# Kernel tuning notes

Hardware: AMD Instinct MI355X
Metric: run time of the kernel (lower is better)

## Reference

```python
import jax, jax.numpy as jnp
import numpy as np

B, S, D, H = 4, 2048, 1024, 16
HD = D // H  # head_dim = 64


def setup_inputs() -> dict:
    key = jax.random.key(0)
    kx, kq, kk, kv, ko = jax.random.split(key, 5)
    scale = 1.0 / np.sqrt(D)
    return {
        "x": jax.random.normal(kx, (B, S, D), dtype=jnp.float32),
        "Wq": jax.random.normal(kq, (D, D), dtype=jnp.float32) * scale,
        "Wk": jax.random.normal(kk, (D, D), dtype=jnp.float32) * scale,
        "Wv": jax.random.normal(kv, (D, D), dtype=jnp.float32) * scale,
        "Wo": jax.random.normal(ko, (D, D), dtype=jnp.float32) * scale,
    }


def reference(x, Wq, Wk, Wv, Wo):
    b, s, d = x.shape
    # torch nn.Linear: y = x @ W.T
    q = (x @ Wq.T).reshape(b, s, H, HD).transpose(0, 2, 1, 3)  # [B,H,S,hd]
    k = (x @ Wk.T).reshape(b, s, H, HD).transpose(0, 2, 1, 3)
    v = (x @ Wv.T).reshape(b, s, H, HD).transpose(0, 2, 1, 3)
    attn = jnp.einsum("bhqd,bhkd->bhqk", q, k) / np.sqrt(HD)  # [B,H,S,S]
    attn = jax.nn.softmax(attn, axis=-1)
    out = jnp.einsum("bhqk,bhkd->bhqd", attn, v)  # [B,H,S,hd]
    per_head = out.transpose(0, 2, 1, 3)  # [B,S,H,hd]
    combined = per_head.reshape(b, s, d)
    projected = combined @ Wo.T
    return projected, per_head
```

## Files before the change

### kernel.cpp

```cpp
#include <hip/hip_runtime.h>
#include <hip/hip_bf16.h>

#define BB 4
#define SS 2048
#define DD 1024
#define HH 16
#define HDD 64
#define MM (BB*SS)

using bf16x8  = __attribute__((ext_vector_type(8))) short;
using f32x4   = __attribute__((ext_vector_type(4))) float;
using f32x16  = __attribute__((ext_vector_type(16))) float;
using ushort8 = __attribute__((ext_vector_type(8))) unsigned short;
using ushort4v= __attribute__((ext_vector_type(4))) unsigned short;
using uint4v  = __attribute__((ext_vector_type(4))) unsigned int;

#if __has_builtin(__builtin_amdgcn_exp2f)
#define EXP2(x) __builtin_amdgcn_exp2f(x)
#else
#define EXP2(x) exp2f(x)
#endif

__device__ __forceinline__ unsigned short f2bf(float x) {
    unsigned u = __builtin_bit_cast(unsigned, x);
    u += 0x7FFFu + ((u >> 16) & 1u);
    return (unsigned short)(u >> 16);
}

__device__ __forceinline__ unsigned int cvtpk(float lo, float hi) {
    unsigned int r;
    asm("v_cvt_pk_bf16_f32 %0, %1, %2" : "=v"(r) : "v"(lo), "v"(hi));
    return r;
}

#define PSWAP(a, b) asm("v_permlane32_swap_b32 %0, %1" : "+v"(a), "+v"(b))

__device__ __forceinline__ void load_lds16(const void* g, void* l) {
    __builtin_amdgcn_global_load_lds(
        (const __attribute__((address_space(1))) void*)g,
        (__attribute__((address_space(3))) void*)l, 16, 0, 0);
}

__global__ __launch_bounds__(256) void cvt_bf16(const float* __restrict__ in,
                                                unsigned short* __restrict__ out,
                                                int n, float scale) {
    int i = (blockIdx.x * 256 + threadIdx.x) * 8;
    if (i >= n) return;
    float4 a = *(const float4*)(in + i);
    float4 b = *(const float4*)(in + i + 4);
    ushort8 r;
    r[0] = f2bf(a.x*scale); r[1] = f2bf(a.y*scale); r[2] = f2bf(a.z*scale); r[3] = f2bf(a.w*scale);
    r[4] = f2bf(b.x*scale); r[5] = f2bf(b.y*scale); r[6] = f2bf(b.z*scale); r[7] = f2bf(b.w*scale);
    *(ushort8*)(out + i) = r;
}

__global__ __launch_bounds__(256) void cvt_weights(const float* __restrict__ wq,
                                                   const float* __restrict__ wk,
                                                   const float* __restrict__ wv,
                                                   const float* __restrict__ wo,
                                                   unsigned short* __restrict__ oq,
                                                   unsigned short* __restrict__ ok,
                                                   unsigned short* __restrict__ ov,
                                                   unsigned short* __restrict__ oo) {
    const int z = blockIdx.y;
    const float* src = z == 0 ? wq : z == 1 ? wk : z == 2 ? wv : wo;
    unsigned short* dst = z == 0 ? oq : z == 1 ? ok : z == 2 ? ov : oo;
    const float scale = z == 0 ? 0.18033688011112042f : 1.0f;
    int i = (blockIdx.x * 256 + threadIdx.x) * 8;
    float4 a = *(const float4*)(src + i);
    float4 b = *(const float4*)(src + i + 4);
    ushort8 r;
    r[0] = f2bf(a.x*scale); r[1] = f2bf(a.y*scale); r[2] = f2bf(a.z*scale); r[3] = f2bf(a.w*scale);
    r[4] = f2bf(b.x*scale); r[5] = f2bf(b.y*scale); r[6] = f2bf(b.z*scale); r[7] = f2bf(b.w*scale);
    *(ushort8*)(dst + i) = r;
}

template<int LAYOUT>
__device__ __forceinline__ void gemm_body(const unsigned short* __restrict__ A,
                                          const unsigned short* __restrict__ W,
                                          void* __restrict__ Cout,
                                          unsigned short* As, unsigned short* Bs) {
    const int t    = threadIdx.x;
    const int lane = t & 63, wid = t >> 6;
    const int wr   = wid >> 1, wc = wid & 1;
    const int lrow = lane & 15, lkg = lane >> 4;
    const int lid  = blockIdx.y * 8 + blockIdx.x;
    const int ord  = (lid & 7) * 64 + (lid >> 3);
    const int row0 = (ord >> 3) * 128, col0 = (ord & 7) * 128;

    f32x4 acc[4][4];
    #pragma unroll
    for (int m = 0; m < 4; ++m)
        #pragma unroll
        for (int n = 0; n < 4; ++n) acc[m][n] = (f32x4){0.f, 0.f, 0.f, 0.f};

    const int c0 = t, c1 = t + 256;
    const unsigned short* Ag0 = A + (size_t)(row0 + (c0 >> 2)) * DD + (c0 & 3) * 8;
    const unsigned short* Ag1 = A + (size_t)(row0 + (c1 >> 2)) * DD + (c1 & 3) * 8;
    const unsigned short* Wg0 = W + (size_t)(col0 + (c0 >> 2)) * DD + (c0 & 3) * 8;
    const unsigned short* Wg1 = W + (size_t)(col0 + (c1 >> 2)) * DD + (c1 & 3) * 8;

    auto stage = [&](int buf, int k0) {
        load_lds16(Ag0 + k0, &As[buf*128*32 + c0 * 8]);
        load_lds16(Ag1 + k0, &As[buf*128*32 + c1 * 8]);
        load_lds16(Wg0 + k0, &Bs[buf*128*32 + c0 * 8]);
        load_lds16(Wg1 + k0, &Bs[buf*128*32 + c1 * 8]);
    };

    stage(0, 0);
    __syncthreads();
    for (int kt = 0; kt < DD / 32; ++kt) {
        const int cur = kt & 1;
        if (kt + 1 < DD / 32) stage(cur ^ 1, (kt + 1) * 32);
        bf16x8 af[4], bfr[4];
        #pragma unroll
        for (int m = 0; m < 4; ++m)
            af[m] = *(const bf16x8*)&As[cur*128*32 + (wr*64 + m*16 + lrow) * 32 + lkg*8];
        #pragma unroll
        for (int n = 0; n < 4; ++n)
            bfr[n] = *(const bf16x8*)&Bs[cur*128*32 + (wc*64 + n*16 + lrow) * 32 + lkg*8];
        __builtin_amdgcn_s_setprio(1);
        #pragma unroll
        for (int m = 0; m < 4; ++m)
            #pragma unroll
            for (int n = 0; n < 4; ++n)
                acc[m][n] = __builtin_amdgcn_mfma_f32_16x16x32_bf16(af[m], bfr[n], acc[m][n], 0, 0, 0);
        __builtin_amdgcn_s_setprio(0);
        __syncthreads();
    }

    #pragma unroll
    for (int m = 0; m < 4; ++m) {
        #pragma unroll
        for (int n = 0; n < 4; ++n) {
            if (LAYOUT == 2) {
                int gm0 = row0 + wr*64 + m*16 + lkg*4;
                int gn  = col0 + wc*64 + n*16 + lrow;
                int b_ = gm0 >> 11, s0 = gm0 & 2047;
                int h_ = gn >> 6,  hd = gn & 63;
                ushort4v hv;
                hv[0] = f2bf(acc[m][n][0]); hv[1] = f2bf(acc[m][n][1]);
                hv[2] = f2bf(acc[m][n][2]); hv[3] = f2bf(acc[m][n][3]);
                *(ushort4v*)&((unsigned short*)Cout)[(((size_t)b_*HH + h_)*HDD + hd)*SS + s0] = hv;
            } else {
                #pragma unroll
                for (int j = 0; j < 4; ++j) {
                    int gm = row0 + wr*64 + m*16 + lkg*4 + j;
                    int gn = col0 + wc*64 + n*16 + lrow;
                    float v = acc[m][n][j];
                    if (LAYOUT == 1) {
                        int b_ = gm >> 11, s_ = gm & 2047;
                        int h_ = gn >> 6,  hd = gn & 63;
                        ((unsigned short*)Cout)[(((size_t)b_*HH + h_)*SS + s_)*HDD + hd] = f2bf(v);
                    } else {
                        ((float*)Cout)[(size_t)gm * DD + gn] = v;
                    }
                }
            }
        }
    }
}

__global__ __launch_bounds__(256) void gemm_qkv(const unsigned short* __restrict__ A,
                                                const unsigned short* __restrict__ Wq,
                                                const unsigned short* __restrict__ Wk,
                                                const unsigned short* __restrict__ Wv,
                                                unsigned short* __restrict__ Q,
                                                unsigned short* __restrict__ K,
                                                unsigned short* __restrict__ V) {
    __shared__ unsigned short As[2*128*32];
    __shared__ unsigned short Bs[2*128*32];
    const int z = blockIdx.z;
    if (z == 2)      gemm_body<2>(A, Wv, V, As, Bs);
    else if (z == 1) gemm_body<1>(A, Wk, K, As, Bs);
    else             gemm_body<1>(A, Wq, Q, As, Bs);
}

__global__ __launch_bounds__(256) void gemm_proj(const unsigned short* __restrict__ A,
                                                 const unsigned short* __restrict__ W,
                                                 float* __restrict__ C) {
    __shared__ unsigned short As[2*128*32];
    __shared__ unsigned short Bs[2*128*32];
    gemm_body<0>(A, W, C, As, Bs);
}

__global__ __launch_bounds__(256, 2) void flash_mfma7(const unsigned short* __restrict__ Qg,
                                                      const unsigned short* __restrict__ Kg,
                                                      const unsigned short* __restrict__ Vtg,
                                                      float* __restrict__ outf,
                                                      unsigned short* __restrict__ outb) {
    __shared__ unsigned short Ks[2][64*64];
    __shared__ unsigned short Vs[2][64*64];
    const int t   = threadIdx.x, lane = t & 63, wid = t >> 6;
    const int l31 = lane & 31;
    const int hi  = lane >> 5;
    const int lid = blockIdx.y * 8 + blockIdx.x;
    const int ord = (lid & 7) * 64 + (lid >> 3);
    const int bh  = ord >> 3, b_ = bh >> 4, h_ = bh & 15;
    const int qA  = (ord & 7) * 256 + wid * 32;

    const unsigned short* Qb = Qg  + (size_t)bh * SS * HDD;
    const unsigned short* Kb = Kg  + (size_t)bh * SS * HDD;
    const unsigned short* Vb = Vtg + (size_t)bh * HDD * SS;

    bf16x8 qfA[4], qfB[4];
    #pragma unroll
    for (int ks = 0; ks < 4; ++ks) {
        qfA[ks] = *(const bf16x8*)&Qb[(size_t)(qA + l31) * HDD + ks*16 + hi*8];
        qfB[ks] = *(const bf16x8*)&Qb[(size_t)(qA + 128 + l31) * HDD + ks*16 + hi*8];
    }

    f32x16 osA0, osA1, osB0, osB1, sumA, sumB, z;
    #pragma unroll
    for (int r = 0; r < 16; ++r) {
        osA0[r] = 0.f; osA1[r] = 0.f; osB0[r] = 0.f; osB1[r] = 0.f;
        sumA[r] = 0.f; sumB[r] = 0.f; z[r] = 0.f;
    }

    bf16x8 onesf;
    #pragma unroll
    for (int e = 0; e < 8; ++e) onesf[e] = (short)0x3F80;

    const int c0 = t, c1 = t + 256;
    const unsigned sb0 = ((unsigned)(c0 << 4)) ^ ((((unsigned)c0 >> 3) & 7u) << 4);
    const unsigned sb1 = ((unsigned)(c1 << 4)) ^ ((((unsigned)c1 >> 3) & 7u) << 4);
    const unsigned xs  = ((unsigned)(l31 & 7)) << 4;

    bf16x8 kr0, kr1, vr0, vr1;
    kr0 = *(const bf16x8*)&Kb[8*c0];
    kr1 = *(const bf16x8*)&Kb[8*c1];
    vr0 = *(const bf16x8*)&Vb[(size_t)(c0 >> 3) * SS + (c0 & 7) * 8];
    vr1 = *(const bf16x8*)&Vb[(size_t)(c1 >> 3) * SS + (c1 & 7) * 8];
    *(bf16x8*)((char*)&Ks[0][0] + sb0) = kr0;
    *(bf16x8*)((char*)&Ks[0][0] + sb1) = kr1;
    *(bf16x8*)((char*)&Vs[0][0] + sb0) = vr0;
    *(bf16x8*)((char*)&Vs[0][0] + sb1) = vr1;
    __syncthreads();

    for (int kt = 0; kt < SS/64; ++kt) {
        const int cur = kt & 1;
        if (kt + 1 < SS/64) {
            kr0 = *(const bf16x8*)&Kb[(size_t)(kt+1)*4096 + 8*c0];
            kr1 = *(const bf16x8*)&Kb[(size_t)(kt+1)*4096 + 8*c1];
            vr0 = *(const bf16x8*)&Vb[(size_t)(c0 >> 3) * SS + (kt+1)*64 + (c0 & 7) * 8];
            vr1 = *(const bf16x8*)&Vb[(size_t)(c1 >> 3) * SS + (kt+1)*64 + (c1 & 7) * 8];
        }
        const char* Kc = (const char*)&Ks[cur][0];
        const char* Vc = (const char*)&Vs[cur][0];

        f32x16 saA0, saA1, saB0, saB1;
        __builtin_amdgcn_s_setprio(1);
        #pragma unroll
        for (int ks = 0; ks < 4; ++ks) {
            const unsigned cb = ks*32 + hi*16;
            bf16x8 kf0 = *(const bf16x8*)(Kc + (((unsigned)(l31*128)      + cb) ^ xs));
            bf16x8 kf1 = *(const bf16x8*)(Kc + (((unsigned)((32+l31)*128) + cb) ^ xs));
            if (ks == 0) {
                saA0 = __builtin_amdgcn_mfma_f32_32x32x16_bf16(kf0, qfA[0], z, 0, 0, 0);
                saA1 = __builtin_amdgcn_mfma_f32_32x32x16_bf16(kf1, qfA[0], z, 0, 0, 0);
                saB0 = __builtin_amdgcn_mfma_f32_32x32x16_bf16(kf0, qfB[0], z, 0, 0, 0);
                saB1 = __builtin_amdgcn_mfma_f32_32x32x16_bf16(kf1, qfB[0], z, 0, 0, 0);
            } else {
                saA0 = __builtin_amdgcn_mfma_f32_32x32x16_bf16(kf0, qfA[ks], saA0, 0, 0, 0);
                saA1 = __builtin_amdgcn_mfma_f32_32x32x16_bf16(kf1, qfA[ks], saA1, 0, 0, 0);
                saB0 = __builtin_amdgcn_mfma_f32_32x32x16_bf16(kf0, qfB[ks], saB0, 0, 0, 0);
                saB1 = __builtin_amdgcn_mfma_f32_32x32x16_bf16(kf1, qfB[ks], saB1, 0, 0, 0);
            }
        }
        __builtin_amdgcn_s_setprio(0);

        unsigned int pkA0[4][2], pkA1[4][2], pkB0[4][2], pkB1[4][2];
        #pragma unroll
        for (int a = 0; a < 4; ++a) {
            #pragma unroll
            for (int h = 0; h < 2; ++h) {
                pkA0[a][h] = cvtpk(EXP2(saA0[4*a + 2*h]), EXP2(saA0[4*a + 2*h + 1]));
                pkA1[a][h] = cvtpk(EXP2(saA1[4*a + 2*h]), EXP2(saA1[4*a + 2*h + 1]));
                pkB0[a][h] = cvtpk(EXP2(saB0[4*a + 2*h]), EXP2(saB0[4*a + 2*h + 1]));
                pkB1[a][h] = cvtpk(EXP2(saB1[4*a + 2*h]), EXP2(saB1[4*a + 2*h + 1]));
            }
        }

        __builtin_amdgcn_s_setprio(1);
        #pragma unroll
        for (int ksg = 0; ksg < 4; ++ksg) {
            const int ks2 = (ksg & 1) * 2;
            unsigned int a0, a1, a2, a3, b0, b1, b2, b3;
            if ((ksg >> 1) == 0) {
                a0 = pkA0[ks2][0]; a2 = pkA0[ks2+1][0]; a1 = pkA0[ks2][1]; a3 = pkA0[ks2+1][1];
                b0 = pkB0[ks2][0]; b2 = pkB0[ks2+1][0]; b1 = pkB0[ks2][1]; b3 = pkB0[ks2+1][1];
            } else {
                a0 = pkA1[ks2][0]; a2 = pkA1[ks2+1][0]; a1 = pkA1[ks2][1]; a3 = pkA1[ks2+1][1];
                b0 = pkB1[ks2][0]; b2 = pkB1[ks2+1][0]; b1 = pkB1[ks2][1]; b3 = pkB1[ks2+1][1];
            }
            PSWAP(a0, a2); PSWAP(a1, a3);
            PSWAP(b0, b2); PSWAP(b1, b3);
            uint4v wa = {a0, a1, a2, a3};
            uint4v wb = {b0, b1, b2, b3};
            bf16x8 pfA = __builtin_bit_cast(bf16x8, wa);
            bf16x8 pfB = __builtin_bit_cast(bf16x8, wb);
            const unsigned cb = ksg*32 + hi*16;
            bf16x8 vf0 = *(const bf16x8*)(Vc + (((unsigned)(l31*128)      + cb) ^ xs));
            bf16x8 vf1 = *(const bf16x8*)(Vc + (((unsigned)((32+l31)*128) + cb) ^ xs));
            osA0 = __builtin_amdgcn_mfma_f32_32x32x16_bf16(vf0, pfA, osA0, 0, 0, 0);
            osA1 = __builtin_amdgcn_mfma_f32_32x32x16_bf16(vf1, pfA, osA1, 0, 0, 0);
            osB0 = __builtin_amdgcn_mfma_f32_32x32x16_bf16(vf0, pfB, osB0, 0, 0, 0);
            osB1 = __builtin_amdgcn_mfma_f32_32x32x16_bf16(vf1, pfB, osB1, 0, 0, 0);
            sumA = __builtin_amdgcn_mfma_f32_32x32x16_bf16(onesf, pfA, sumA, 0, 0, 0);
            sumB = __builtin_amdgcn_mfma_f32_32x32x16_bf16(onesf, pfB, sumB, 0, 0, 0);
        }
        __builtin_amdgcn_s_setprio(0);

        if (kt + 1 < SS/64) {
            char* Kn = (char*)&Ks[cur ^ 1][0];
            char* Vn = (char*)&Vs[cur ^ 1][0];
            *(bf16x8*)(Kn + sb0) = kr0;
            *(bf16x8*)(Kn + sb1) = kr1;
            *(bf16x8*)(Vn + sb0) = vr0;
            *(bf16x8*)(Vn + sb1) = vr1;
        }
        __syncthreads();
    }

    #pragma unroll
    for (int g = 0; g < 2; ++g) {
        const float invl = 1.0f / (g == 0 ? sumA[0] : sumB[0]);
        const int   s_   = qA + (g ? 128 : 0) + l31;
        float*          po = outf + (((size_t)b_ * SS + s_) * HH + h_) * HDD;
        unsigned short* pb = outb + (((size_t)b_ * SS + s_) * HH + h_) * HDD;
        #pragma unroll
        for (int a = 0; a < 4; ++a) {
            {
                const f32x16& o = g == 0 ? osA0 : osB0;
                const int d0 = 8*a + 4*hi;
                float4 v; v.x = o[4*a+0]*invl; v.y = o[4*a+1]*invl;
                          v.z = o[4*a+2]*invl; v.w = o[4*a+3]*invl;
                *(float4*)&po[d0] = v;
                ushort4v hv; hv[0]=f2bf(v.x); hv[1]=f2bf(v.y); hv[2]=f2bf(v.z); hv[3]=f2bf(v.w);
                *(ushort4v*)&pb[d0] = hv;
            }
            {
                const f32x16& o = g == 0 ? osA1 : osB1;
                const int d0 = 32 + 8*a + 4*hi;
                float4 v; v.x = o[4*a+0]*invl; v.y = o[4*a+1]*invl;
                          v.z = o[4*a+2]*invl; v.w = o[4*a+3]*invl;
                *(float4*)&po[d0] = v;
                ushort4v hv; hv[0]=f2bf(v.x); hv[1]=f2bf(v.y); hv[2]=f2bf(v.z); hv[3]=f2bf(v.w);
                *(ushort4v*)&pb[d0] = hv;
            }
        }
    }
}

extern "C" void kernel_launch(void* const* d_in, const int* in_sizes, int n_in,
                              void* d_out, int out_size, void* d_ws, size_t ws_size,
                              hipStream_t stream) {
    const float* x  = (const float*)d_in[0];
    const float* Wq = (const float*)d_in[1];
    const float* Wk = (const float*)d_in[2];
    const float* Wv = (const float*)d_in[3];
    const float* Wo = (const float*)d_in[4];
    float* out      = (float*)d_out;
    float* per_head = out + (size_t)MM * DD;

    unsigned short* ws   = (unsigned short*)d_ws;
    const size_t NE = (size_t)MM * DD;
    unsigned short* Qbf  = ws;
    unsigned short* Kbf  = Qbf + NE;
    unsigned short* Vbf  = Kbf + NE;
    unsigned short* xbf  = Vbf + NE;
    unsigned short* wqbf = xbf + NE;
    unsigned short* wkbf = wqbf + (size_t)DD * DD;
    unsigned short* wvbf = wkbf + (size_t)DD * DD;
    unsigned short* wobf = wvbf + (size_t)DD * DD;
    unsigned short* cbf  = wobf + (size_t)DD * DD;

    const int nx = MM * DD;
    const int nw = DD * DD;
    cvt_bf16<<<nx / 2048, 256, 0, stream>>>(x, xbf, nx, 1.0f);
    cvt_weights<<<dim3(nw / 2048, 4), 256, 0, stream>>>(Wq, Wk, Wv, Wo,
                                                        wqbf, wkbf, wvbf, wobf);

    gemm_qkv<<<dim3(DD / 128, MM / 128, 3), 256, 0, stream>>>(xbf, wqbf, wkbf, wvbf,
                                                              Qbf, Kbf, Vbf);

    flash_mfma7<<<dim3(8, BB * HH), 256, 0, stream>>>(Qbf, Kbf, Vbf, per_head, cbf);

    gemm_proj<<<dim3(DD / 128, MM / 128), 256, 0, stream>>>(cbf, wobf, out);
}
```

Baseline: 192.8 us.

## Double flash K/V tile to 128 keys, merge conversion kernels, pack bf16 stores

The flash attention kernel now stages 128 keys of K and V per iteration instead of 64 and processes them as two 64-key halves. This halves the number of barriers and global-to-LDS round trips, at the cost of twice the LDS (64 KB per block), which may limit occupancy at two blocks per CU. The x and weight conversion kernels are merged into one launch. The bf16 output stores now use the packed hardware convert instruction.

Measured after the change: 207.1 us. +7.4%, slower.

```diff
diff --git a/kernel.cpp b/kernel.cpp
--- a/kernel.cpp
+++ b/kernel.cpp
@@ -13,6 +13,7 @@
 using f32x16  = __attribute__((ext_vector_type(16))) float;
 using ushort8 = __attribute__((ext_vector_type(8))) unsigned short;
 using ushort4v= __attribute__((ext_vector_type(4))) unsigned short;
+using uint2v  = __attribute__((ext_vector_type(2))) unsigned int;
 using uint4v  = __attribute__((ext_vector_type(4))) unsigned int;
 
 #if __has_builtin(__builtin_amdgcn_exp2f)
@@ -41,32 +42,27 @@
         (__attribute__((address_space(3))) void*)l, 16, 0, 0);
 }
 
-__global__ __launch_bounds__(256) void cvt_bf16(const float* __restrict__ in,
-                                                unsigned short* __restrict__ out,
-                                                int n, float scale) {
-    int i = (blockIdx.x * 256 + threadIdx.x) * 8;
-    if (i >= n) return;
-    float4 a = *(const float4*)(in + i);
-    float4 b = *(const float4*)(in + i + 4);
-    ushort8 r;
-    r[0] = f2bf(a.x*scale); r[1] = f2bf(a.y*scale); r[2] = f2bf(a.z*scale); r[3] = f2bf(a.w*scale);
-    r[4] = f2bf(b.x*scale); r[5] = f2bf(b.y*scale); r[6] = f2bf(b.z*scale); r[7] = f2bf(b.w*scale);
-    *(ushort8*)(out + i) = r;
-}
-
-__global__ __launch_bounds__(256) void cvt_weights(const float* __restrict__ wq,
-                                                   const float* __restrict__ wk,
-                                                   const float* __restrict__ wv,
-                                                   const float* __restrict__ wo,
-                                                   unsigned short* __restrict__ oq,
-                                                   unsigned short* __restrict__ ok,
-                                                   unsigned short* __restrict__ ov,
-                                                   unsigned short* __restrict__ oo) {
+__global__ __launch_bounds__(256) void cvt_all(const float* __restrict__ x,
+                                               const float* __restrict__ wq,
+                                               const float* __restrict__ wk,
+                                               const float* __restrict__ wv,
+                                               const float* __restrict__ wo,
+                                               unsigned short* __restrict__ ox,
+                                               unsigned short* __restrict__ oq,
+                                               unsigned short* __restrict__ ok,
+                                               unsigned short* __restrict__ ov,
+                                               unsigned short* __restrict__ oo) {
     const int z = blockIdx.y;
-    const float* src = z == 0 ? wq : z == 1 ? wk : z == 2 ? wv : wo;
-    unsigned short* dst = z == 0 ? oq : z == 1 ? ok : z == 2 ? ov : oo;
-    const float scale = z == 0 ? 0.18033688011112042f : 1.0f;
-    int i = (blockIdx.x * 256 + threadIdx.x) * 8;
+    const float* src;
+    unsigned short* dst;
+    float scale = 1.0f;
+    size_t base;
+    if (z < 8)       { src = x;  dst = ox; base = (size_t)z * 512 * 2048; }
+    else if (z == 8) { src = wq; dst = oq; base = 0; scale = 0.18033688011112042f; }
+    else if (z == 9) { src = wk; dst = ok; base = 0; }
+    else if (z == 10){ src = wv; dst = ov; base = 0; }
+    else             { src = wo; dst = oo; base = 0; }
+    size_t i = base + ((size_t)blockIdx.x * 256 + threadIdx.x) * 8;
     float4 a = *(const float4*)(src + i);
     float4 b = *(const float4*)(src + i + 4);
     ushort8 r;
@@ -184,13 +180,13 @@
     gemm_body<0>(A, W, C, As, Bs);
 }
 
-__global__ __launch_bounds__(256, 2) void flash_mfma7(const unsigned short* __restrict__ Qg,
+__global__ __launch_bounds__(256, 2) void flash_mfma8(const unsigned short* __restrict__ Qg,
                                                       const unsigned short* __restrict__ Kg,
                                                       const unsigned short* __restrict__ Vtg,
                                                       float* __restrict__ outf,
                                                       unsigned short* __restrict__ outb) {
-    __shared__ unsigned short Ks[2][64*64];
-    __shared__ unsigned short Vs[2][64*64];
+    __shared__ unsigned short Ks[2][128*64];
+    __shared__ unsigned short Vs[2][2*64*64];
     const int t   = threadIdx.x, lane = t & 63, wid = t >> 6;
     const int l31 = lane & 31;
     const int hi  = lane >> 5;
@@ -221,103 +217,118 @@
     #pragma unroll
     for (int e = 0; e < 8; ++e) onesf[e] = (short)0x3F80;
 
-    const int c0 = t, c1 = t + 256;
-    const unsigned sb0 = ((unsigned)(c0 << 4)) ^ ((((unsigned)c0 >> 3) & 7u) << 4);
-    const unsigned sb1 = ((unsigned)(c1 << 4)) ^ ((((unsigned)c1 >> 3) & 7u) << 4);
-    const unsigned xs  = ((unsigned)(l31 & 7)) << 4;
-
-    bf16x8 kr0, kr1, vr0, vr1;
-    kr0 = *(const bf16x8*)&Kb[8*c0];
-    kr1 = *(const bf16x8*)&Kb[8*c1];
-    vr0 = *(const bf16x8*)&Vb[(size_t)(c0 >> 3) * SS + (c0 & 7) * 8];
-    vr1 = *(const bf16x8*)&Vb[(size_t)(c1 >> 3) * SS + (c1 & 7) * 8];
-    *(bf16x8*)((char*)&Ks[0][0] + sb0) = kr0;
-    *(bf16x8*)((char*)&Ks[0][0] + sb1) = kr1;
-    *(bf16x8*)((char*)&Vs[0][0] + sb0) = vr0;
-    *(bf16x8*)((char*)&Vs[0][0] + sb1) = vr1;
+    unsigned sbK[4], sbV[4];
+    const unsigned short* Kg4[4];
+    const unsigned short* Vg4[4];
+    #pragma unroll
+    for (int i = 0; i < 4; ++i) {
+        const int c = t + 256*i;
+        sbK[i] = ((unsigned)(c << 4)) ^ ((((unsigned)c >> 3) & 7u) << 4);
+        const int half = c >> 9, cv = c & 511;
+        sbV[i] = (unsigned)(half * 8192)
+               + (((unsigned)(cv << 4)) ^ ((((unsigned)cv >> 3) & 7u) << 4));
+        Kg4[i] = Kb + 8*c;
+        Vg4[i] = Vb + (size_t)(cv >> 3) * SS + half*64 + (cv & 7) * 8;
+    }
+    const unsigned xs = ((unsigned)(l31 & 7)) << 4;
+
+    bf16x8 kr[4], vr[4];
+    #pragma unroll
+    for (int i = 0; i < 4; ++i) {
+        kr[i] = *(const bf16x8*)Kg4[i];
+        vr[i] = *(const bf16x8*)Vg4[i];
+        *(bf16x8*)((char*)&Ks[0][0] + sbK[i]) = kr[i];
+        *(bf16x8*)((char*)&Vs[0][0] + sbV[i]) = vr[i];
+    }
     __syncthreads();
 
-    for (int kt = 0; kt < SS/64; ++kt) {
+    for (int kt = 0; kt < SS/128; ++kt) {
         const int cur = kt & 1;
-        if (kt + 1 < SS/64) {
-            kr0 = *(const bf16x8*)&Kb[(size_t)(kt+1)*4096 + 8*c0];
-            kr1 = *(const bf16x8*)&Kb[(size_t)(kt+1)*4096 + 8*c1];
-            vr0 = *(const bf16x8*)&Vb[(size_t)(c0 >> 3) * SS + (kt+1)*64 + (c0 & 7) * 8];
-            vr1 = *(const bf16x8*)&Vb[(size_t)(c1 >> 3) * SS + (kt+1)*64 + (c1 & 7) * 8];
-        }
-        const char* Kc = (const char*)&Ks[cur][0];
-        const char* Vc = (const char*)&Vs[cur][0];
-
-        f32x16 saA0, saA1, saB0, saB1;
-        __builtin_amdgcn_s_setprio(1);
-        #pragma unroll
-        for (int ks = 0; ks < 4; ++ks) {
-            const unsigned cb = ks*32 + hi*16;
-            bf16x8 kf0 = *(const bf16x8*)(Kc + (((unsigned)(l31*128)      + cb) ^ xs));
-            bf16x8 kf1 = *(const bf16x8*)(Kc + (((unsigned)((32+l31)*128) + cb) ^ xs));
-            if (ks == 0) {
-                saA0 = __builtin_amdgcn_mfma_f32_32x32x16_bf16(kf0, qfA[0], z, 0, 0, 0);
-                saA1 = __builtin_amdgcn_mfma_f32_32x32x16_bf16(kf1, qfA[0], z, 0, 0, 0);
-                saB0 = __builtin_amdgcn_mfma_f32_32x32x16_bf16(kf0, qfB[0], z, 0, 0, 0);
-                saB1 = __builtin_amdgcn_mfma_f32_32x32x16_bf16(kf1, qfB[0], z, 0, 0, 0);
-            } else {
-                saA0 = __builtin_amdgcn_mfma_f32_32x32x16_bf16(kf0, qfA[ks], saA0, 0, 0, 0);
-                saA1 = __builtin_amdgcn_mfma_f32_32x32x16_bf16(kf1, qfA[ks], saA1, 0, 0, 0);
-                saB0 = __builtin_amdgcn_mfma_f32_32x32x16_bf16(kf0, qfB[ks], saB0, 0, 0, 0);
-                saB1 = __builtin_amdgcn_mfma_f32_32x32x16_bf16(kf1, qfB[ks], saB1, 0, 0, 0);
-            }
-        }
-        __builtin_amdgcn_s_setprio(0);
-
-        unsigned int pkA0[4][2], pkA1[4][2], pkB0[4][2], pkB1[4][2];
-        #pragma unroll
-        for (int a = 0; a < 4; ++a) {
-            #pragma unroll
-            for (int h = 0; h < 2; ++h) {
-                pkA0[a][h] = cvtpk(EXP2(saA0[4*a + 2*h]), EXP2(saA0[4*a + 2*h + 1]));
-                pkA1[a][h] = cvtpk(EXP2(saA1[4*a + 2*h]), EXP2(saA1[4*a + 2*h + 1]));
-                pkB0[a][h] = cvtpk(EXP2(saB0[4*a + 2*h]), EXP2(saB0[4*a + 2*h + 1]));
-                pkB1[a][h] = cvtpk(EXP2(saB1[4*a + 2*h]), EXP2(saB1[4*a + 2*h + 1]));
-            }
-        }
-
-        __builtin_amdgcn_s_setprio(1);
-        #pragma unroll
-        for (int ksg = 0; ksg < 4; ++ksg) {
-            const int ks2 = (ksg & 1) * 2;
-            unsigned int a0, a1, a2, a3, b0, b1, b2, b3;
-            if ((ksg >> 1) == 0) {
-                a0 = pkA0[ks2][0]; a2 = pkA0[ks2+1][0]; a1 = pkA0[ks2][1]; a3 = pkA0[ks2+1][1];
-                b0 = pkB0[ks2][0]; b2 = pkB0[ks2+1][0]; b1 = pkB0[ks2][1]; b3 = pkB0[ks2+1][1];
-            } else {
-                a0 = pkA1[ks2][0]; a2 = pkA1[ks2+1][0]; a1 = pkA1[ks2][1]; a3 = pkA1[ks2+1][1];
-                b0 = pkB1[ks2][0]; b2 = pkB1[ks2+1][0]; b1 = pkB1[ks2][1]; b3 = pkB1[ks2+1][1];
-            }
-            PSWAP(a0, a2); PSWAP(a1, a3);
-            PSWAP(b0, b2); PSWAP(b1, b3);
-            uint4v wa = {a0, a1, a2, a3};
-            uint4v wb = {b0, b1, b2, b3};
-            bf16x8 pfA = __builtin_bit_cast(bf16x8, wa);
-            bf16x8 pfB = __builtin_bit_cast(bf16x8, wb);
-            const unsigned cb = ksg*32 + hi*16;
-            bf16x8 vf0 = *(const bf16x8*)(Vc + (((unsigned)(l31*128)      + cb) ^ xs));
-            bf16x8 vf1 = *(const bf16x8*)(Vc + (((unsigned)((32+l31)*128) + cb) ^ xs));
-            osA0 = __builtin_amdgcn_mfma_f32_32x32x16_bf16(vf0, pfA, osA0, 0, 0, 0);
-            osA1 = __builtin_amdgcn_mfma_f32_32x32x16_bf16(vf1, pfA, osA1, 0, 0, 0);
-            osB0 = __builtin_amdgcn_mfma_f32_32x32x16_bf16(vf0, pfB, osB0, 0, 0, 0);
-            osB1 = __builtin_amdgcn_mfma_f32_32x32x16_bf16(vf1, pfB, osB1, 0, 0, 0);
-            sumA = __builtin_amdgcn_mfma_f32_32x32x16_bf16(onesf, pfA, sumA, 0, 0, 0);
-            sumB = __builtin_amdgcn_mfma_f32_32x32x16_bf16(onesf, pfB, sumB, 0, 0, 0);
-        }
-        __builtin_amdgcn_s_setprio(0);
-
-        if (kt + 1 < SS/64) {
+        if (kt + 1 < SS/128) {
+            #pragma unroll
+            for (int i = 0; i < 4; ++i) {
+                kr[i] = *(const bf16x8*)(Kg4[i] + (size_t)(kt+1)*8192);
+                vr[i] = *(const bf16x8*)(Vg4[i] + (kt+1)*128);
+            }
+        }
+
+        #pragma unroll
+        for (int h2 = 0; h2 < 2; ++h2) {
+            const char* Kc = (const char*)&Ks[cur][0] + h2 * 8192;
+            const char* Vc = (const char*)&Vs[cur][0] + h2 * 8192;
+
+            f32x16 saA0, saA1, saB0, saB1;
+            __builtin_amdgcn_s_setprio(1);
+            #pragma unroll
+            for (int ks = 0; ks < 4; ++ks) {
+                const unsigned cb = ks*32 + hi*16;
+                bf16x8 kf0 = *(const bf16x8*)(Kc + (((unsigned)(l31*128)      + cb) ^ xs));
+                bf16x8 kf1 = *(const bf16x8*)(Kc + (((unsigned)((32+l31)*128) + cb) ^ xs));
+                if (ks == 0) {
+                    saA0 = __builtin_amdgcn_mfma_f32_32x32x16_bf16(kf0, qfA[0], z, 0, 0, 0);
+                    saA1 = __builtin_amdgcn_mfma_f32_32x32x16_bf16(kf1, qfA[0], z, 0, 0, 0);
+                    saB0 = __builtin_amdgcn_mfma_f32_32x32x16_bf16(kf0, qfB[0], z, 0, 0, 0);
+                    saB1 = __builtin_amdgcn_mfma_f32_32x32x16_bf16(kf1, qfB[0], z, 0, 0, 0);
+                } else {
+                    saA0 = __builtin_amdgcn_mfma_f32_32x32x16_bf16(kf0, qfA[ks], saA0, 0, 0, 0);
+                    saA1 = __builtin_amdgcn_mfma_f32_32x32x16_bf16(kf1, qfA[ks], saA1, 0, 0, 0);
+                    saB0 = __builtin_amdgcn_mfma_f32_32x32x16_bf16(kf0, qfB[ks], saB0, 0, 0, 0);
+                    saB1 = __builtin_amdgcn_mfma_f32_32x32x16_bf16(kf1, qfB[ks], saB1, 0, 0, 0);
+                }
+            }
+            __builtin_amdgcn_s_setprio(0);
+
+            unsigned int pkA0[4][2], pkA1[4][2], pkB0[4][2], pkB1[4][2];
+            #pragma unroll
+            for (int a = 0; a < 4; ++a) {
+                #pragma unroll
+                for (int h = 0; h < 2; ++h) {
+                    pkA0[a][h] = cvtpk(EXP2(saA0[4*a + 2*h]), EXP2(saA0[4*a + 2*h + 1]));
+                    pkA1[a][h] = cvtpk(EXP2(saA1[4*a + 2*h]), EXP2(saA1[4*a + 2*h + 1]));
+                    pkB0[a][h] = cvtpk(EXP2(saB0[4*a + 2*h]), EXP2(saB0[4*a + 2*h + 1]));
+                    pkB1[a][h] = cvtpk(EXP2(saB1[4*a + 2*h]), EXP2(saB1[4*a + 2*h + 1]));
+                }
+            }
+
+            __builtin_amdgcn_s_setprio(1);
+            #pragma unroll
+            for (int ksg = 0; ksg < 4; ++ksg) {
+                const int ks2 = (ksg & 1) * 2;
+                unsigned int a0, a1, a2, a3, b0, b1, b2, b3;
+                if ((ksg >> 1) == 0) {
+                    a0 = pkA0[ks2][0]; a2 = pkA0[ks2+1][0]; a1 = pkA0[ks2][1]; a3 = pkA0[ks2+1][1];
+                    b0 = pkB0[ks2][0]; b2 = pkB0[ks2+1][0]; b1 = pkB0[ks2][1]; b3 = pkB0[ks2+1][1];
+                } else {
+                    a0 = pkA1[ks2][0]; a2 = pkA1[ks2+1][0]; a1 = pkA1[ks2][1]; a3 = pkA1[ks2+1][1];
+                    b0 = pkB1[ks2][0]; b2 = pkB1[ks2+1][0]; b1 = pkB1[ks2][1]; b3 = pkB1[ks2+1][1];
+                }
+                PSWAP(a0, a2); PSWAP(a1, a3);
+                PSWAP(b0, b2); PSWAP(b1, b3);
+                uint4v wa = {a0, a1, a2, a3};
+                uint4v wb = {b0, b1, b2, b3};
+                bf16x8 pfA = __builtin_bit_cast(bf16x8, wa);
+                bf16x8 pfB = __builtin_bit_cast(bf16x8, wb);
+                const unsigned cb = ksg*32 + hi*16;
+                bf16x8 vf0 = *(const bf16x8*)(Vc + (((unsigned)(l31*128)      + cb) ^ xs));
+                bf16x8 vf1 = *(const bf16x8*)(Vc + (((unsigned)((32+l31)*128) + cb) ^ xs));
+                osA0 = __builtin_amdgcn_mfma_f32_32x32x16_bf16(vf0, pfA, osA0, 0, 0, 0);
+                osA1 = __builtin_amdgcn_mfma_f32_32x32x16_bf16(vf1, pfA, osA1, 0, 0, 0);
+                osB0 = __builtin_amdgcn_mfma_f32_32x32x16_bf16(vf0, pfB, osB0, 0, 0, 0);
+                osB1 = __builtin_amdgcn_mfma_f32_32x32x16_bf16(vf1, pfB, osB1, 0, 0, 0);
+                sumA = __builtin_amdgcn_mfma_f32_32x32x16_bf16(onesf, pfA, sumA, 0, 0, 0);
+                sumB = __builtin_amdgcn_mfma_f32_32x32x16_bf16(onesf, pfB, sumB, 0, 0, 0);
+            }
+            __builtin_amdgcn_s_setprio(0);
+        }
+
+        if (kt + 1 < SS/128) {
             char* Kn = (char*)&Ks[cur ^ 1][0];
             char* Vn = (char*)&Vs[cur ^ 1][0];
-            *(bf16x8*)(Kn + sb0) = kr0;
-            *(bf16x8*)(Kn + sb1) = kr1;
-            *(bf16x8*)(Vn + sb0) = vr0;
-            *(bf16x8*)(Vn + sb1) = vr1;
+            #pragma unroll
+            for (int i = 0; i < 4; ++i) {
+                *(bf16x8*)(Kn + sbK[i]) = kr[i];
+                *(bf16x8*)(Vn + sbV[i]) = vr[i];
+            }
         }
         __syncthreads();
     }
@@ -336,8 +347,8 @@
                 float4 v; v.x = o[4*a+0]*invl; v.y = o[4*a+1]*invl;
                           v.z = o[4*a+2]*invl; v.w = o[4*a+3]*invl;
                 *(float4*)&po[d0] = v;
-                ushort4v hv; hv[0]=f2bf(v.x); hv[1]=f2bf(v.y); hv[2]=f2bf(v.z); hv[3]=f2bf(v.w);
-                *(ushort4v*)&pb[d0] = hv;
+                uint2v hv; hv[0] = cvtpk(v.x, v.y); hv[1] = cvtpk(v.z, v.w);
+                *(uint2v*)&pb[d0] = hv;
             }
             {
                 const f32x16& o = g == 0 ? osA1 : osB1;
@@ -345,8 +356,8 @@
                 float4 v; v.x = o[4*a+0]*invl; v.y = o[4*a+1]*invl;
                           v.z = o[4*a+2]*invl; v.w = o[4*a+3]*invl;
                 *(float4*)&po[d0] = v;
-                ushort4v hv; hv[0]=f2bf(v.x); hv[1]=f2bf(v.y); hv[2]=f2bf(v.z); hv[3]=f2bf(v.w);
-                *(ushort4v*)&pb[d0] = hv;
+                uint2v hv; hv[0] = cvtpk(v.x, v.y); hv[1] = cvtpk(v.z, v.w);
+                *(uint2v*)&pb[d0] = hv;
             }
         }
     }
@@ -375,16 +386,13 @@
     unsigned short* wobf = wvbf + (size_t)DD * DD;
     unsigned short* cbf  = wobf + (size_t)DD * DD;
 
-    const int nx = MM * DD;
-    const int nw = DD * DD;
-    cvt_bf16<<<nx / 2048, 256, 0, stream>>>(x, xbf, nx, 1.0f);
-    cvt_weights<<<dim3(nw / 2048, 4), 256, 0, stream>>>(Wq, Wk, Wv, Wo,
-                                                        wqbf, wkbf, wvbf, wobf);
+    cvt_all<<<dim3(512, 12), 256, 0, stream>>>(x, Wq, Wk, Wv, Wo,
+                                               xbf, wqbf, wkbf, wvbf, wobf);
 
     gemm_qkv<<<dim3(DD / 128, MM / 128, 3), 256, 0, stream>>>(xbf, wqbf, wkbf, wvbf,
                                                               Qbf, Kbf, Vbf);
 
-    flash_mfma7<<<dim3(8, BB * HH), 256, 0, stream>>>(Qbf, Kbf, Vbf, per_head, cbf);
+    flash_mfma8<<<dim3(8, BB * HH), 256, 0, stream>>>(Qbf, Kbf, Vbf, per_head, cbf);
 
     gemm_proj<<<dim3(DD / 128, MM / 128), 256, 0, stream>>>(cbf, wobf, out);
 }
```
